# Performance work log

Measured on AMD Instinct MI355X. Metric: run time of the kernel, lower is better.

Reference implementation:

```python
import jax, jax.numpy as jnp
import numpy as np

B, N = 8, 1024
C = [256, 512, 1024]
C2 = C[1]
KV = sum(C)            # 1792
H = 4                  # num_attention_heads
EXPAND = 4
LN_EPS = 1e-6
IN_EPS = 1e-5          # nn.InstanceNorm2d default eps


def setup_inputs() -> dict:
    key = jax.random.key(0)
    ks = jax.random.split(key, 16)
    s = 0.02
    inp = {
        "emb1": jax.random.normal(ks[0], (B, N, C[0]), jnp.float32),
        "emb2": jax.random.normal(ks[1], (B, N, C[1]), jnp.float32),
        "emb3": jax.random.normal(ks[2], (B, N, C[2]), jnp.float32),
        # per-head projection weights stored as [in, out] (torch Linear applies x @ W.T)
        "Wq": jax.random.normal(ks[3], (H, C2, C2), jnp.float32) * s,
        "Wk": jax.random.normal(ks[4], (H, KV, KV), jnp.float32) * s,
        "Wv": jax.random.normal(ks[5], (H, KV, KV), jnp.float32) * s,
        "Wout": jax.random.normal(ks[6], (C2, C2), jnp.float32) * s,
        "ln1_g": jnp.ones((C2,), jnp.float32),
        "ln1_b": jnp.zeros((C2,), jnp.float32),
        "lnall_g": jnp.ones((KV,), jnp.float32),
        "lnall_b": jnp.zeros((KV,), jnp.float32),
        "lnffn_g": jnp.ones((C2,), jnp.float32),
        "lnffn_b": jnp.zeros((C2,), jnp.float32),
        "fc1_w": jax.random.normal(ks[7], (C2, C2 * EXPAND), jnp.float32) * s,
        "fc1_b": jnp.zeros((C2 * EXPAND,), jnp.float32),
        "fc2_w": jax.random.normal(ks[8], (C2 * EXPAND, C2), jnp.float32) * s,
        "fc2_b": jnp.zeros((C2,), jnp.float32),
    }
    return inp


def _layer_norm(x, g, b, eps=LN_EPS):
    m = jnp.mean(x, axis=-1, keepdims=True)
    v = jnp.var(x, axis=-1, keepdims=True)
    return (x - m) * jax.lax.rsqrt(v + eps) * g + b


def _instance_norm2d(x, eps=IN_EPS):
    # x: [B, H, C2, KV]; normalize each (B,H) map over its last two dims (no affine)
    m = jnp.mean(x, axis=(-2, -1), keepdims=True)
    v = jnp.var(x, axis=(-2, -1), keepdims=True)
    return (x - m) * jax.lax.rsqrt(v + eps)


def reference(emb1, emb2, emb3, Wq, Wk, Wv, Wout,
              ln1_g, ln1_b, lnall_g, lnall_b, lnffn_g, lnffn_b,
              fc1_w, fc1_b, fc2_w, fc2_b):
    org2 = emb2
    emb_all = jnp.concatenate([emb1, emb2, emb3], axis=2)        # [B,N,KV]
    cx2 = _layer_norm(emb2, ln1_g, ln1_b)                         # [B,N,C2]
    emb_all = _layer_norm(emb_all, lnall_g, lnall_b)              # [B,N,KV]

    # batched per-head projections (replaces the Python ModuleList loop)
    q = jnp.einsum('bnc,hcd->bhnd', cx2, Wq)                      # [B,H,N,C2]
    k = jnp.einsum('bnc,hcd->bhnd', emb_all, Wk)                  # [B,H,N,KV]
    v = jnp.einsum('bnc,hcd->bhnd', emb_all, Wv)                  # [B,H,N,KV]

    # channel attention: q^T k over the token axis
    scores = jnp.einsum('bhnc,bhnk->bhck', q, k) / np.sqrt(KV)    # [B,H,C2,KV]
    probs = jax.nn.softmax(_instance_norm2d(scores), axis=3)      # [B,H,C2,KV]

    # context = probs @ v^T, then mean over heads (fused into one einsum)
    ctx = jnp.einsum('bhck,bhnk->bnc', probs, v) / H              # [B,N,C2]
    o = ctx @ Wout                                                # [B,N,C2]

    cx2 = org2 + o
    x2 = _layer_norm(cx2, lnffn_g, lnffn_b)
    x2 = jax.nn.gelu(x2 @ fc1_w + fc1_b, approximate=False)
    x2 = x2 @ fc2_w + fc2_b
    return x2 + cx2
```

## Files before the change

### kernel.cpp

```cpp
#include <hip/hip_runtime.h>
#include <cstdint>
#include <cmath>

typedef __bf16 bf16_t;
typedef __attribute__((ext_vector_type(8))) __bf16 bf16x8;
typedef __attribute__((ext_vector_type(4))) float f32x4;

#define AS_G(x) ((__attribute__((address_space(1))) void*)(x))
#define AS_L(x) ((__attribute__((address_space(3))) void*)(x))

#define BK 64

#define BSZ 8
#define NTOK 1024
#define CC2 512
#define KVD 1792
#define NH 4
#define FFD 2048
#define ROWS 8192

#define BARM()   asm volatile("s_barrier" ::: "memory")
#define VMCNT8() asm volatile("s_waitcnt vmcnt(8)" ::: "memory")
#define VMCNT4() asm volatile("s_waitcnt vmcnt(4)" ::: "memory")
#define VMCNT0() asm volatile("s_waitcnt vmcnt(0)" ::: "memory")
#define LGKMD()  asm volatile("s_waitcnt lgkmcnt(0)" ::: "memory")


__device__ __forceinline__ void stage_pair(const bf16_t* __restrict__ A,
                                           const bf16_t* __restrict__ B,
                                           int ld, bf16_t* ldsA, bf16_t* ldsB, int tid)
{
#pragma unroll
  for (int it = 0; it < 4; ++it) {
    int chunk = it * 256 + tid;
    int r = chunk >> 3;
    int s = chunk & 7;
    int cg = ((s ^ (r & 7)) << 3);
    __builtin_amdgcn_global_load_lds(AS_G(A + (long)r * ld + cg),
                                     AS_L(ldsA + chunk * 8), 16, 0, 0);
    __builtin_amdgcn_global_load_lds(AS_G(B + (long)r * ld + cg),
                                     AS_L(ldsB + chunk * 8), 16, 0, 0);
  }
}

__device__ __forceinline__ void mfma_step(const bf16_t* ldsA, const bf16_t* ldsB,
                                          f32x4 acc[4][4], int wr, int wc, int lane, int kc)
{
  const int quad = lane >> 4, l16 = lane & 15;
  bf16x8 a[4], b[4];
#pragma unroll
  for (int i = 0; i < 4; ++i) {
    int r = wr * 64 + i * 16 + l16;
    int slot = (kc + quad) ^ (r & 7);
    a[i] = *(const bf16x8*)(ldsA + r * BK + slot * 8);
  }
#pragma unroll
  for (int j = 0; j < 4; ++j) {
    int r = wc * 64 + j * 16 + l16;
    int slot = (kc + quad) ^ (r & 7);
    b[j] = *(const bf16x8*)(ldsB + r * BK + slot * 8);
  }
#pragma unroll
  for (int i = 0; i < 4; ++i)
#pragma unroll
    for (int j = 0; j < 4; ++j)
      acc[i][j] = __builtin_amdgcn_mfma_f32_16x16x32_bf16(a[i], b[j], acc[i][j], 0, 0, 0);
}

#define GEMM_PROLOG() \
  __shared__ __align__(16) bf16_t ldsA[2][128 * BK]; \
  __shared__ __align__(16) bf16_t ldsB[2][128 * BK]; \
  const int tid = threadIdx.x; \
  const int wave = tid >> 6, lane = tid & 63; \
  const int wr = wave >> 1, wc = wave & 1; \
  f32x4 acc[4][4] = {};

#define GEMM_LOOP(Aptr, Bptr, Kdim) { \
  const bf16_t* Ap_ = (Aptr); const bf16_t* Bp_ = (Bptr); const int Kd_ = (Kdim); \
  const int nt_ = Kd_ / BK; \
  stage_pair(Ap_, Bp_, Kd_, ldsA[0], ldsB[0], tid); \
  for (int t = 0; t < nt_; ++t) { \
    const int cur = t & 1; \
    if (t + 1 < nt_) { \
      stage_pair(Ap_ + (t + 1) * BK, Bp_ + (t + 1) * BK, Kd_, ldsA[cur ^ 1], ldsB[cur ^ 1], tid); \
      VMCNT8(); \
    } else { VMCNT0(); } \
    BARM(); \
    mfma_step(ldsA[cur], ldsB[cur], acc, wr, wc, lane, 0); \
    mfma_step(ldsA[cur], ldsB[cur], acc, wr, wc, lane, 4); \
    LGKMD(); \
    BARM(); \
  } }

template <typename F>
__device__ __forceinline__ void epilogue_apply(f32x4 acc[4][4], int wr, int wc, int lane, F f)
{
  const int quad = lane >> 4, l16 = lane & 15;
#pragma unroll
  for (int i = 0; i < 4; ++i)
#pragma unroll
    for (int j = 0; j < 4; ++j)
#pragma unroll
      for (int r = 0; r < 4; ++r)
        f(wr * 64 + i * 16 + quad * 4 + r, wc * 64 + j * 16 + l16, acc[i][j][r]);
}


__device__ __forceinline__ void stage256h(const bf16_t* __restrict__ A,
                                          const bf16_t* __restrict__ B,
                                          int ld, bf16_t* ldsA, bf16_t* ldsB, int tid, int h)
{
#pragma unroll
  for (int i = 0; i < 2; ++i) {
    int it = h * 2 + i;
    int chunk = it * 512 + tid;
    int r = chunk >> 3;
    int s = chunk & 7;
    int cg = ((s ^ (r & 7)) << 3);
    __builtin_amdgcn_global_load_lds(AS_G(A + (long)r * ld + cg),
                                     AS_L(ldsA + chunk * 8), 16, 0, 0);
    __builtin_amdgcn_global_load_lds(AS_G(B + (long)r * ld + cg),
                                     AS_L(ldsB + chunk * 8), 16, 0, 0);
  }
}

__device__ __forceinline__ void qread_a(const bf16_t* ldsOp, int wr, int rh, int lane,
                                        bf16x8 a[4][2])
{
  const int quad = lane >> 4, l16 = lane & 15;
#pragma unroll
  for (int mi = 0; mi < 4; ++mi)
#pragma unroll
    for (int kc = 0; kc < 2; ++kc) {
      int r = wr * 128 + rh * 64 + mi * 16 + l16;
      int slot = (kc * 4 + quad) ^ (r & 7);
      a[mi][kc] = *(const bf16x8*)(ldsOp + r * BK + slot * 8);
    }
}

__device__ __forceinline__ void qread_b(const bf16_t* ldsOp, int wc, int ch, int lane,
                                        bf16x8 b[2][2])
{
  const int quad = lane >> 4, l16 = lane & 15;
#pragma unroll
  for (int nj = 0; nj < 2; ++nj)
#pragma unroll
    for (int kc = 0; kc < 2; ++kc) {
      int r = wc * 64 + ch * 32 + nj * 16 + l16;
      int slot = (kc * 4 + quad) ^ (r & 7);
      b[nj][kc] = *(const bf16x8*)(ldsOp + r * BK + slot * 8);
    }
}

template <int RH, int CH>
__device__ __forceinline__ void mfma16(f32x4 acc[8][4], const bf16x8 a[4][2],
                                       const bf16x8 (&b)[2][2])
{
#pragma unroll
  for (int mi = 0; mi < 4; ++mi)
#pragma unroll
    for (int nj = 0; nj < 2; ++nj)
#pragma unroll
      for (int kc = 0; kc < 2; ++kc)
        acc[RH * 4 + mi][CH * 2 + nj] =
            __builtin_amdgcn_mfma_f32_16x16x32_bf16(a[mi][kc], b[nj][kc],
                                                    acc[RH * 4 + mi][CH * 2 + nj], 0, 0, 0);
}

#define GEMM256_PROLOG() \
  __shared__ __align__(16) bf16_t ldsA[2][256 * BK]; \
  __shared__ __align__(16) bf16_t ldsB[2][256 * BK]; \
  __shared__ float sred[16]; \
  (void)sred; \
  const int tid = threadIdx.x; \
  const int wave = tid >> 6, lane = tid & 63; \
  const int wr = wave >> 2, wc = wave & 3; \
  f32x4 acc[8][4] = {};

#define GEMM256_LOOP(Aptr, Bptr, Kdim) { \
  const bf16_t* Ap = (Aptr); const bf16_t* Bp = (Bptr); const int Kd = (Kdim); \
  const int nt = Kd / BK; \
  stage256h(Ap, Bp, Kd, ldsA[0], ldsB[0], tid, 0); \
  stage256h(Ap, Bp, Kd, ldsA[0], ldsB[0], tid, 1); \
  for (int t = 0; t < nt; ++t) { \
    const int cur = t & 1; \
    if (t + 1 < nt) { \
      stage256h(Ap + (t + 1) * BK, Bp + (t + 1) * BK, Kd, ldsA[cur ^ 1], ldsB[cur ^ 1], tid, 0); \
      VMCNT4(); \
    } else { VMCNT0(); } \
    BARM(); \
    { \
      bf16x8 a[4][2], b0[2][2], b1[2][2]; \
      qread_a(ldsA[cur], wr, 0, lane, a); \
      qread_b(ldsB[cur], wc, 0, lane, b0); \
      qread_b(ldsB[cur], wc, 1, lane, b1); \
      mfma16<0, 0>(acc, a, b0); \
      mfma16<0, 1>(acc, a, b1); \
      if (t + 1 < nt) \
        stage256h(Ap + (t + 1) * BK, Bp + (t + 1) * BK, Kd, ldsA[cur ^ 1], ldsB[cur ^ 1], tid, 1); \
      qread_a(ldsA[cur], wr, 1, lane, a); \
      mfma16<1, 0>(acc, a, b0); \
      mfma16<1, 1>(acc, a, b1); \
    } \
    LGKMD(); \
    BARM(); \
  } }

template <typename F>
__device__ __forceinline__ void epi256(f32x4 acc[8][4], int wr, int wc, int lane, F f)
{
  const int quad = lane >> 4, l16 = lane & 15;
#pragma unroll
  for (int i = 0; i < 8; ++i)
#pragma unroll
    for (int j = 0; j < 4; ++j)
#pragma unroll
      for (int r = 0; r < 4; ++r)
        f(wr * 128 + (i >> 2) * 64 + (i & 3) * 16 + quad * 4 + r,
          wc * 64 + (j >> 1) * 32 + (j & 1) * 16 + l16, acc[i][j][r]);
}

__device__ __forceinline__ void swzA(int mg, int& bx, int& by, int& bz)
{
  int lid = blockIdx.x + 2 * (blockIdx.y + 7 * blockIdx.z);
  int xcd = lid & 7, s = lid >> 3;
  int y = s % 7, t = s / 7;
  bx = t & 1;
  by = y;
  if (mg) bz = (xcd >> 1) * 8 + (xcd & 1) * 4 + (t >> 1);
  else    bz = (xcd >> 2) * 8 + (xcd & 3) * 2 + (t >> 1);
}


__global__ void zstats_k(float* s)
{
  if (threadIdx.x < 64) s[threadIdx.x] = 0.f;
}

__global__ __launch_bounds__(256) void tconv_k(const float* __restrict__ in,
                                               bf16_t* __restrict__ out, int R, int Cc)
{
  __shared__ float tile[32][33];
  const long base = (long)blockIdx.z * R * Cc;
  const int c0 = blockIdx.x * 32, r0 = blockIdx.y * 32;
  const int tx = threadIdx.x & 31, ty = threadIdx.x >> 5;
#pragma unroll
  for (int i = 0; i < 4; ++i)
    tile[ty + i * 8][tx] = in[base + (long)(r0 + ty + i * 8) * Cc + c0 + tx];
  __syncthreads();
#pragma unroll
  for (int i = 0; i < 4; ++i)
    out[base + (long)(c0 + ty + i * 8) * R + r0 + tx] = (bf16_t)tile[tx][ty + i * 8];
}

__global__ __launch_bounds__(256) void tconv_bf_k(const bf16_t* __restrict__ in,
                                                  bf16_t* __restrict__ out, int R, int Cc)
{
  __shared__ float tile[32][33];
  const long base = (long)blockIdx.z * R * Cc;
  const int c0 = blockIdx.x * 32, r0 = blockIdx.y * 32;
  const int tx = threadIdx.x & 31, ty = threadIdx.x >> 5;
#pragma unroll
  for (int i = 0; i < 4; ++i)
    tile[ty + i * 8][tx] = (float)in[base + (long)(r0 + ty + i * 8) * Cc + c0 + tx];
  __syncthreads();
#pragma unroll
  for (int i = 0; i < 4; ++i)
    out[base + (long)(c0 + ty + i * 8) * R + r0 + tx] = (bf16_t)tile[tx][ty + i * 8];
}

__global__ __launch_bounds__(256) void cast_k(const float* __restrict__ in,
                                              bf16_t* __restrict__ out, long n)
{
  long i = ((long)blockIdx.x * 256 + threadIdx.x) * 4;
  if (i + 3 < n) {
    float4 v = *(const float4*)(in + i);
    out[i] = (bf16_t)v.x; out[i + 1] = (bf16_t)v.y;
    out[i + 2] = (bf16_t)v.z; out[i + 3] = (bf16_t)v.w;
  }
}

__global__ __launch_bounds__(256) void msum_add_k(const bf16_t* __restrict__ M,
                                                  bf16_t* __restrict__ O, int nfold)
{
  const long SLICE = (long)8 * CC2 * KVD;
  long i = ((long)blockIdx.x * 256 + threadIdx.x) * 8;
  float acc[8] = {};
  for (int h = 0; h < nfold; ++h) {
    bf16x8 x = *(const bf16x8*)(M + h * SLICE + i);
#pragma unroll
    for (int j = 0; j < 8; ++j) acc[j] += (float)x[j];
  }
  bf16x8 r;
#pragma unroll
  for (int j = 0; j < 8; ++j) r[j] = (bf16_t)acc[j];
  *(bf16x8*)(O + i) = r;
}

__global__ __launch_bounds__(256) void ln_concat_k(const float* __restrict__ e1,
                                                   const float* __restrict__ e2,
                                                   const float* __restrict__ e3,
                                                   const float* __restrict__ g1,
                                                   const float* __restrict__ b1,
                                                   const float* __restrict__ ga,
                                                   const float* __restrict__ ba,
                                                   bf16_t* __restrict__ cxln,
                                                   bf16_t* __restrict__ embln)
{
  const long row = blockIdx.x;
  const float* p1 = e1 + row * 256;
  const float* p2 = e2 + row * 512;
  const float* p3 = e3 + row * 1024;
  const int t = threadIdx.x;
  float vals[7];
  float sa = 0.f, qa = 0.f;
#pragma unroll
  for (int i = 0; i < 7; ++i) {
    int idx = t + i * 256;
    float x = (idx < 256) ? p1[idx] : (idx < 768 ? p2[idx - 256] : p3[idx - 768]);
    vals[i] = x;
    sa += x; qa += x * x;
  }
  float s2 = vals[1] + vals[2];
  float q2 = vals[1] * vals[1] + vals[2] * vals[2];
  for (int off = 32; off; off >>= 1) {
    sa += __shfl_down(sa, off, 64); qa += __shfl_down(qa, off, 64);
    s2 += __shfl_down(s2, off, 64); q2 += __shfl_down(q2, off, 64);
  }
  __shared__ float red[4][4];
  const int wave = t >> 6, lane = t & 63;
  if (lane == 0) { red[0][wave] = sa; red[1][wave] = qa; red[2][wave] = s2; red[3][wave] = q2; }
  __syncthreads();
  float SA = red[0][0] + red[0][1] + red[0][2] + red[0][3];
  float QA = red[1][0] + red[1][1] + red[1][2] + red[1][3];
  float S2 = red[2][0] + red[2][1] + red[2][2] + red[2][3];
  float Q2 = red[3][0] + red[3][1] + red[3][2] + red[3][3];
  float ma = SA * (1.f / 1792.f);
  float va = QA * (1.f / 1792.f) - ma * ma;
  float rsa = rsqrtf(va + 1e-6f);
  float m2 = S2 * (1.f / 512.f);
  float v2 = Q2 * (1.f / 512.f) - m2 * m2;
  float rs2 = rsqrtf(v2 + 1e-6f);
#pragma unroll
  for (int i = 0; i < 7; ++i) {
    int idx = t + i * 256;
    embln[row * 1792 + idx] = (bf16_t)((vals[i] - ma) * rsa * ga[idx] + ba[idx]);
  }
  cxln[row * 512 + t]       = (bf16_t)((vals[1] - m2) * rs2 * g1[t] + b1[t]);
  cxln[row * 512 + t + 256] = (bf16_t)((vals[2] - m2) * rs2 * g1[t + 256] + b1[t + 256]);
}

__global__ __launch_bounds__(256) void ln2_k(const float* __restrict__ X,
                                             const float* __restrict__ g,
                                             const float* __restrict__ bb,
                                             bf16_t* __restrict__ Y)
{
  const long row = blockIdx.x;
  const float* p = X + row * 512;
  const int t = threadIdx.x;
  float x0 = p[t], x1 = p[t + 256];
  float s = x0 + x1, q = x0 * x0 + x1 * x1;
  for (int off = 32; off; off >>= 1) {
    s += __shfl_down(s, off, 64); q += __shfl_down(q, off, 64);
  }
  __shared__ float red[2][4];
  const int wave = t >> 6, lane = t & 63;
  if (lane == 0) { red[0][wave] = s; red[1][wave] = q; }
  __syncthreads();
  float S = red[0][0] + red[0][1] + red[0][2] + red[0][3];
  float Q = red[1][0] + red[1][1] + red[1][2] + red[1][3];
  float m = S * (1.f / 512.f);
  float v = Q * (1.f / 512.f) - m * m;
  float rs = rsqrtf(v + 1e-6f);
  Y[row * 512 + t]       = (bf16_t)((x0 - m) * rs * g[t] + bb[t]);
  Y[row * 512 + t + 256] = (bf16_t)((x1 - m) * rs * g[t + 256] + bb[t + 256]);
}

__global__ __launch_bounds__(256) void softmax_k(bf16_t* __restrict__ SC,
                                                 const float* __restrict__ stats)
{
  const long rowid = blockIdx.x;
  const int z = (int)(rowid >> 9);
  const float inv_cnt = 1.f / (512.f * 1792.f);
  float m = stats[2 * z] * inv_cnt;
  float var = stats[2 * z + 1] * inv_cnt - m * m;
  float rs = rsqrtf(var + 1e-5f);
  bf16_t* rowp = SC + rowid * 1792;
  const int t = threadIdx.x;
  float v[7];
  float mx = -1e30f;
#pragma unroll
  for (int i = 0; i < 7; ++i) {
    v[i] = (float)rowp[t + i * 256] * rs;
    mx = fmaxf(mx, v[i]);
  }
  for (int off = 32; off; off >>= 1) mx = fmaxf(mx, __shfl_down(mx, off, 64));
  __shared__ float red[8];
  const int wave = t >> 6, lane = t & 63;
  if (lane == 0) red[wave] = mx;
  __syncthreads();
  mx = fmaxf(fmaxf(red[0], red[1]), fmaxf(red[2], red[3]));
  float sum = 0.f;
#pragma unroll
  for (int i = 0; i < 7; ++i) { v[i] = __expf(v[i] - mx); sum += v[i]; }
  for (int off = 32; off; off >>= 1) sum += __shfl_down(sum, off, 64);
  if (lane == 0) red[4 + wave] = sum;
  __syncthreads();
  float inv = 1.f / (red[4] + red[5] + red[6] + red[7]);
#pragma unroll
  for (int i = 0; i < 7; ++i) rowp[t + i * 256] = (bf16_t)(v[i] * inv);
}


__global__ __launch_bounds__(256) void gemm_ab(const bf16_t* __restrict__ A, long astride,
                                               const bf16_t* __restrict__ B, long bstride,
                                               bf16_t* __restrict__ C, long cstride,
                                               int K, int ldc)
{
  const int z = blockIdx.z;
  GEMM_PROLOG();
  const bf16_t* Ap = A + z * astride + (long)blockIdx.x * 128 * K;
  const bf16_t* Bp = B + z * bstride + (long)blockIdx.y * 128 * K;
  GEMM_LOOP(Ap, Bp, K);
  bf16_t* Cb = C + (long)z * cstride;
  const int rbase = blockIdx.x * 128, cbase = blockIdx.y * 128;
  epilogue_apply(acc, wr, wc, lane, [&](int rr, int cc, float v) {
    Cb[(long)(rbase + rr) * ldc + cbase + cc] = (bf16_t)v;
  });
}

__global__ __launch_bounds__(512, 2) void gemm_t1_256(const bf16_t* __restrict__ WqT,
                                                      const bf16_t* __restrict__ Gt,
                                                      bf16_t* __restrict__ T1, int mg)
{
  int bxx, byy, bzz;
  swzA(mg, bxx, byy, bzz);
  const int z = bzz, hh = z >> 3, b = z & 7;
  GEMM256_PROLOG();
  const bf16_t* Ap0 = WqT + (long)hh * CC2 * CC2 + (long)bxx * 256 * CC2;
  const bf16_t* Bp0 = Gt + (long)b * KVD * CC2 + (long)byy * 256 * CC2;
  GEMM256_LOOP(Ap0, Bp0, CC2);
  bf16_t* Cb = T1 + (long)z * CC2 * KVD;
  const int rbase = bxx * 256, cbase = byy * 256;
  epi256(acc, wr, wc, lane, [&](int rr, int cc, float v) {
    Cb[(long)(rbase + rr) * KVD + cbase + cc] = (bf16_t)v;
  });
}

__global__ __launch_bounds__(512, 2) void gemm_scores_256(const bf16_t* __restrict__ T1,
                                                          const bf16_t* __restrict__ WkT,
                                                          bf16_t* __restrict__ SC,
                                                          float* __restrict__ stats, int mg)
{
  int bxx, byy, bzz;
  swzA(mg, bxx, byy, bzz);
  const int z = bzz, hh = z >> 3;
  GEMM256_PROLOG();
  const bf16_t* Ap0 = T1 + (long)z * CC2 * KVD + (long)bxx * 256 * KVD;
  const bf16_t* Bp0 = WkT + (long)hh * KVD * KVD + (long)byy * 256 * KVD;
  GEMM256_LOOP(Ap0, Bp0, KVD);
  const float scale = 0.02362277854f;
  bf16_t* Cb = SC + (long)z * CC2 * KVD;
  const int rbase = bxx * 256, cbase = byy * 256;
  float s = 0.f, q = 0.f;
  epi256(acc, wr, wc, lane, [&](int rr, int cc, float v) {
    v *= scale;
    Cb[(long)(rbase + rr) * KVD + cbase + cc] = (bf16_t)v;
    s += v; q += v * v;
  });
  for (int off = 32; off; off >>= 1) { s += __shfl_down(s, off, 64); q += __shfl_down(q, off, 64); }
  if (lane == 0) { sred[wave] = s; sred[8 + wave] = q; }
  __syncthreads();
  if (tid == 0) {
    float S = 0.f, Q = 0.f;
#pragma unroll
    for (int w = 0; w < 8; ++w) { S += sred[w]; Q += sred[8 + w]; }
    atomicAdd(&stats[2 * z], S);
    atomicAdd(&stats[2 * z + 1], Q);
  }
}

__global__ __launch_bounds__(512, 2) void gemm_macc_256(const bf16_t* __restrict__ P,
                                                        const bf16_t* __restrict__ WvB,
                                                        bf16_t* __restrict__ M,
                                                        int first, int mg)
{
  int bxx, byy, bzz;
  swzA(mg, bxx, byy, bzz);
  const int z = bzz, hh = z >> 3;
  GEMM256_PROLOG();
  const bf16_t* Ap0 = P + (long)z * CC2 * KVD + (long)bxx * 256 * KVD;
  const bf16_t* Bp0 = WvB + (long)hh * KVD * KVD + (long)byy * 256 * KVD;
  GEMM256_LOOP(Ap0, Bp0, KVD);
  bf16_t* Cb = M + (long)z * CC2 * KVD;
  const int rbase = bxx * 256, cbase = byy * 256;
  epi256(acc, wr, wc, lane, [&](int rr, int cc, float v) {
    long idx = (long)(rbase + rr) * KVD + cbase + cc;
    float prev = first ? 0.f : (float)Cb[idx];
    Cb[idx] = (bf16_t)(prev + v * 0.25f);
  });
}

__global__ __launch_bounds__(256) void gemm_ctx(const bf16_t* __restrict__ E,
                                                const bf16_t* __restrict__ Msum8,
                                                bf16_t* __restrict__ CTX)
{
  const int b = blockIdx.z;
  GEMM_PROLOG();
  const bf16_t* Ap = E + (long)b * NTOK * KVD + (long)blockIdx.x * 128 * KVD;
  const bf16_t* Bp = Msum8 + (long)b * CC2 * KVD + (long)blockIdx.y * 128 * KVD;
  GEMM_LOOP(Ap, Bp, KVD);
  bf16_t* Cb = CTX + (long)b * NTOK * CC2;
  const int rbase = blockIdx.x * 128, cbase = blockIdx.y * 128;
  epilogue_apply(acc, wr, wc, lane, [&](int rr, int cc, float v) {
    Cb[(long)(rbase + rr) * CC2 + cbase + cc] = (bf16_t)v;
  });
}

__global__ __launch_bounds__(256) void gemm_resid(const bf16_t* __restrict__ A,
                                                  const bf16_t* __restrict__ B,
                                                  const float* __restrict__ emb2,
                                                  float* __restrict__ CX2)
{
  GEMM_PROLOG();
  const bf16_t* Ap = A + (long)blockIdx.x * 128 * CC2;
  const bf16_t* Bp = B + (long)blockIdx.y * 128 * CC2;
  GEMM_LOOP(Ap, Bp, CC2);
  const int rbase = blockIdx.x * 128, cbase = blockIdx.y * 128;
  epilogue_apply(acc, wr, wc, lane, [&](int rr, int cc, float v) {
    long idx = (long)(rbase + rr) * CC2 + cbase + cc;
    CX2[idx] = v + emb2[idx];
  });
}

__global__ __launch_bounds__(512, 2) void gemm_gelu_256(const bf16_t* __restrict__ A,
                                                        const bf16_t* __restrict__ B,
                                                        const float* __restrict__ bias,
                                                        bf16_t* __restrict__ H)
{
  GEMM256_PROLOG();
  const bf16_t* Ap0 = A + (long)blockIdx.x * 256 * CC2;
  const bf16_t* Bp0 = B + (long)blockIdx.y * 256 * CC2;
  GEMM256_LOOP(Ap0, Bp0, CC2);
  const int rbase = blockIdx.x * 256, cbase = blockIdx.y * 256;
  epi256(acc, wr, wc, lane, [&](int rr, int cc, float v) {
    float x = v + bias[cbase + cc];
    float g = 0.5f * x * (1.0f + erff(x * 0.70710678118f));
    H[(long)(rbase + rr) * FFD + cbase + cc] = (bf16_t)g;
  });
}

__global__ __launch_bounds__(256) void gemm_out(const bf16_t* __restrict__ A,
                                                const bf16_t* __restrict__ B,
                                                const float* __restrict__ bias,
                                                const float* __restrict__ CX2,
                                                float* __restrict__ OUT)
{
  GEMM_PROLOG();
  const bf16_t* Ap = A + (long)blockIdx.x * 128 * FFD;
  const bf16_t* Bp = B + (long)blockIdx.y * 128 * FFD;
  GEMM_LOOP(Ap, Bp, FFD);
  const int rbase = blockIdx.x * 128, cbase = blockIdx.y * 128;
  epilogue_apply(acc, wr, wc, lane, [&](int rr, int cc, float v) {
    long idx = (long)(rbase + rr) * CC2 + cbase + cc;
    OUT[idx] = v + bias[cbase + cc] + CX2[idx];
  });
}


extern "C" void kernel_launch(void* const* d_in, const int* in_sizes, int n_in,
                              void* d_out, int out_size, void* d_ws, size_t ws_size,
                              hipStream_t stream)
{
  const float* emb1   = (const float*)d_in[0];
  const float* emb2   = (const float*)d_in[1];
  const float* emb3   = (const float*)d_in[2];
  const float* Wq     = (const float*)d_in[3];
  const float* Wk     = (const float*)d_in[4];
  const float* Wv     = (const float*)d_in[5];
  const float* Wout   = (const float*)d_in[6];
  const float* ln1_g  = (const float*)d_in[7];
  const float* ln1_b  = (const float*)d_in[8];
  const float* lnall_g = (const float*)d_in[9];
  const float* lnall_b = (const float*)d_in[10];
  const float* lnffn_g = (const float*)d_in[11];
  const float* lnffn_b = (const float*)d_in[12];
  const float* fc1_w  = (const float*)d_in[13];
  const float* fc1_b  = (const float*)d_in[14];
  const float* fc2_w  = (const float*)d_in[15];
  const float* fc2_b  = (const float*)d_in[16];
  float* out = (float*)d_out;
  (void)in_sizes; (void)n_in; (void)out_size;

  const bool merged = ws_size >= (size_t)306 * 1000 * 1000;
  const int nheads = merged ? 4 : 2;
  const int nz = merged ? 32 : 16;
  const int nmslot = merged ? 32 : 16;

  char* ws = (char*)d_ws;
  size_t off = 0;
  auto alloc = [&](size_t bytes) {
    size_t r = off;
    off = (off + bytes + 255) & ~(size_t)255;
    return r;
  };

  size_t oEMBLN = alloc((size_t)ROWS * KVD * 2);
  size_t oCXLN  = alloc((size_t)ROWS * CC2 * 2);
  size_t oCX2   = alloc((size_t)ROWS * CC2 * 4);
  size_t oGt    = alloc((size_t)BSZ * KVD * CC2 * 2);
  size_t oMsum  = alloc((size_t)nmslot * CC2 * KVD * 2);
  size_t oWOT   = alloc((size_t)CC2 * CC2 * 2);
  size_t oF1T   = alloc((size_t)FFD * CC2 * 2);
  size_t oF2T   = alloc((size_t)CC2 * FFD * 2);
  size_t oSTATS = alloc(64 * 4);
  size_t oSCR   = alloc(0);
  size_t oCXLNT  = alloc((size_t)BSZ * CC2 * NTOK * 2);
  size_t oEMBLNT = alloc((size_t)BSZ * KVD * NTOK * 2);

  bf16_t* EMBLN  = (bf16_t*)(ws + oEMBLN);
  bf16_t* CXLN   = (bf16_t*)(ws + oCXLN);
  float*  CX2    = (float*)(ws + oCX2);
  bf16_t* Gt     = (bf16_t*)(ws + oGt);
  bf16_t* Msum   = (bf16_t*)(ws + oMsum);
  bf16_t* WOT    = (bf16_t*)(ws + oWOT);
  bf16_t* F1T    = (bf16_t*)(ws + oF1T);
  bf16_t* F2T    = (bf16_t*)(ws + oF2T);
  float*  STATS  = (float*)(ws + oSTATS);
  bf16_t* CXLNT  = (bf16_t*)(ws + oCXLNT);
  bf16_t* EMBLNT = (bf16_t*)(ws + oEMBLNT);

  char* scr = ws + oSCR;
  auto rnd = [](size_t v) { return (v + 255) & ~(size_t)255; };
  bf16_t* WqT = (bf16_t*)(scr);
  bf16_t* WkT = (bf16_t*)(scr + rnd((size_t)nheads * CC2 * CC2 * 2));
  bf16_t* WvB = (bf16_t*)((char*)WkT + rnd((size_t)nheads * KVD * KVD * 2));
  bf16_t* T1  = (bf16_t*)((char*)WvB + rnd((size_t)nheads * KVD * KVD * 2));
  bf16_t* SC  = (bf16_t*)((char*)T1 + rnd((size_t)nz * CC2 * KVD * 2));
  bf16_t* Msum8 = (bf16_t*)(scr);
  bf16_t* CTX   = (bf16_t*)(scr + rnd((size_t)8 * CC2 * KVD * 2));
  bf16_t* FFNH  = (bf16_t*)((char*)CTX + rnd((size_t)ROWS * CC2 * 2));
  bf16_t* X2LN = CXLN;

  zstats_k<<<1, 64, 0, stream>>>(STATS);
  tconv_k<<<dim3(16, 16), 256, 0, stream>>>(Wout, WOT, 512, 512);
  tconv_k<<<dim3(64, 16), 256, 0, stream>>>(fc1_w, F1T, 512, 2048);
  tconv_k<<<dim3(16, 64), 256, 0, stream>>>(fc2_w, F2T, 2048, 512);

  ln_concat_k<<<8192, 256, 0, stream>>>(emb1, emb2, emb3, ln1_g, ln1_b,
                                        lnall_g, lnall_b, CXLN, EMBLN);

  tconv_bf_k<<<dim3(16, 32, 8), 256, 0, stream>>>(CXLN, CXLNT, 1024, 512);
  tconv_bf_k<<<dim3(56, 32, 8), 256, 0, stream>>>(EMBLN, EMBLNT, 1024, 1792);
  gemm_ab<<<dim3(14, 4, 8), 256, 0, stream>>>(EMBLNT, (long)KVD * NTOK,
                                              CXLNT, (long)CC2 * NTOK,
                                              Gt, (long)KVD * CC2, NTOK, CC2);

  if (merged) {
    tconv_k<<<dim3(16, 16, 4), 256, 0, stream>>>(Wq, WqT, 512, 512);
    tconv_k<<<dim3(56, 56, 4), 256, 0, stream>>>(Wk, WkT, 1792, 1792);
    cast_k<<<12544, 256, 0, stream>>>(Wv, WvB, (long)4 * KVD * KVD);

    gemm_t1_256<<<dim3(2, 7, 32), 512, 0, stream>>>(WqT, Gt, T1, 1);
    gemm_scores_256<<<dim3(2, 7, 32), 512, 0, stream>>>(T1, WkT, SC, STATS, 1);
    softmax_k<<<16384, 256, 0, stream>>>(SC, STATS);
    gemm_macc_256<<<dim3(2, 7, 32), 512, 0, stream>>>(SC, WvB, Msum, 1, 1);
    msum_add_k<<<3584, 256, 0, stream>>>(Msum, Msum8, 4);
  } else {
    for (int g = 0; g < 2; ++g) {
      tconv_k<<<dim3(16, 16, 2), 256, 0, stream>>>(Wq + (long)g * 2 * CC2 * CC2, WqT, 512, 512);
      tconv_k<<<dim3(56, 56, 2), 256, 0, stream>>>(Wk + (long)g * 2 * KVD * KVD, WkT, 1792, 1792);
      cast_k<<<6272, 256, 0, stream>>>(Wv + (long)g * 2 * KVD * KVD, WvB, (long)2 * KVD * KVD);

      gemm_t1_256<<<dim3(2, 7, 16), 512, 0, stream>>>(WqT, Gt, T1, 0);
      gemm_scores_256<<<dim3(2, 7, 16), 512, 0, stream>>>(T1, WkT, SC, STATS + g * 32, 0);
      softmax_k<<<8192, 256, 0, stream>>>(SC, STATS + g * 32);
      gemm_macc_256<<<dim3(2, 7, 16), 512, 0, stream>>>(SC, WvB, Msum, g == 0 ? 1 : 0, 0);
    }
    msum_add_k<<<3584, 256, 0, stream>>>(Msum, Msum8, 2);
  }

  gemm_ctx<<<dim3(8, 4, 8), 256, 0, stream>>>(EMBLN, Msum8, CTX);

  gemm_resid<<<dim3(64, 4), 256, 0, stream>>>(CTX, WOT, emb2, CX2);

  ln2_k<<<8192, 256, 0, stream>>>(CX2, lnffn_g, lnffn_b, X2LN);
  gemm_gelu_256<<<dim3(32, 8), 512, 0, stream>>>(X2LN, F1T, fc1_b, FFNH);
  gemm_out<<<dim3(64, 4), 256, 0, stream>>>(FFNH, F2T, fc2_b, CX2, out);
}
```

Measured before the change: 745.3 us.

## Fuse softmax normalization into value GEMM A-operand loading

The softmax kernel now only computes per-row max and inverse sum and stores them in a small side buffer. The exponentiation and normalization are applied to the A fragments inside the macc GEMM after they are read from LDS. This removes a full write pass over the score matrix. In exchange it adds exp work inside the GEMM inner loop, recomputed for every column tile, plus register pressure from the per-row stats.

```diff
diff --git a/kernel.cpp b/kernel.cpp
--- a/kernel.cpp
+++ b/kernel.cpp
@@ -165,6 +165,18 @@
         acc[RH * 4 + mi][CH * 2 + nj] =
             __builtin_amdgcn_mfma_f32_16x16x32_bf16(a[mi][kc], b[nj][kc],
                                                     acc[RH * 4 + mi][CH * 2 + nj], 0, 0, 0);
+}
+
+__device__ __forceinline__ void pexp(bf16x8 a[4][2], const float* mxr, const float* invr,
+                                     float rs)
+{
+#pragma unroll
+  for (int mi = 0; mi < 4; ++mi)
+#pragma unroll
+    for (int kc = 0; kc < 2; ++kc)
+#pragma unroll
+      for (int j = 0; j < 8; ++j)
+        a[mi][kc][j] = (bf16_t)(__expf((float)a[mi][kc][j] * rs - mxr[mi]) * invr[mi]);
 }
 
 #define GEMM256_PROLOG() \
@@ -376,8 +388,9 @@
   Y[row * 512 + t + 256] = (bf16_t)((x1 - m) * rs * g[t + 256] + bb[t + 256]);
 }
 
-__global__ __launch_bounds__(256) void softmax_k(bf16_t* __restrict__ SC,
-                                                 const float* __restrict__ stats)
+__global__ __launch_bounds__(256) void sstats_k(const bf16_t* __restrict__ SC,
+                                                const float* __restrict__ stats,
+                                                float* __restrict__ srow)
 {
   const long rowid = blockIdx.x;
   const int z = (int)(rowid >> 9);
@@ -385,7 +398,7 @@
   float m = stats[2 * z] * inv_cnt;
   float var = stats[2 * z + 1] * inv_cnt - m * m;
   float rs = rsqrtf(var + 1e-5f);
-  bf16_t* rowp = SC + rowid * 1792;
+  const bf16_t* rowp = SC + rowid * 1792;
   const int t = threadIdx.x;
   float v[7];
   float mx = -1e30f;
@@ -402,13 +415,14 @@
   mx = fmaxf(fmaxf(red[0], red[1]), fmaxf(red[2], red[3]));
   float sum = 0.f;
 #pragma unroll
-  for (int i = 0; i < 7; ++i) { v[i] = __expf(v[i] - mx); sum += v[i]; }
+  for (int i = 0; i < 7; ++i) sum += __expf(v[i] - mx);
   for (int off = 32; off; off >>= 1) sum += __shfl_down(sum, off, 64);
   if (lane == 0) red[4 + wave] = sum;
   __syncthreads();
-  float inv = 1.f / (red[4] + red[5] + red[6] + red[7]);
-#pragma unroll
-  for (int i = 0; i < 7; ++i) rowp[t + i * 256] = (bf16_t)(v[i] * inv);
+  if (t == 0) {
+    srow[rowid * 2]     = mx;
+    srow[rowid * 2 + 1] = 1.f / (red[4] + red[5] + red[6] + red[7]);
+  }
 }
 
 
@@ -482,6 +496,8 @@
 
 __global__ __launch_bounds__(512, 2) void gemm_macc_256(const bf16_t* __restrict__ P,
                                                         const bf16_t* __restrict__ WvB,
+                                                        const float* __restrict__ stats,
+                                                        const float* __restrict__ srow,
                                                         bf16_t* __restrict__ M,
                                                         int first, int mg)
 {
@@ -489,9 +505,50 @@
   swzA(mg, bxx, byy, bzz);
   const int z = bzz, hh = z >> 3;
   GEMM256_PROLOG();
-  const bf16_t* Ap0 = P + (long)z * CC2 * KVD + (long)bxx * 256 * KVD;
-  const bf16_t* Bp0 = WvB + (long)hh * KVD * KVD + (long)byy * 256 * KVD;
-  GEMM256_LOOP(Ap0, Bp0, KVD);
+  const float inv_cnt = 1.f / (512.f * 1792.f);
+  float sm = stats[2 * z] * inv_cnt;
+  float var = stats[2 * z + 1] * inv_cnt - sm * sm;
+  float rs = rsqrtf(var + 1e-5f);
+  const int ll16 = lane & 15;
+  float mxr[2][4], invr[2][4];
+#pragma unroll
+  for (int rh = 0; rh < 2; ++rh)
+#pragma unroll
+    for (int mi = 0; mi < 4; ++mi) {
+      long rr = (long)z * 512 + bxx * 256 + wr * 128 + rh * 64 + mi * 16 + ll16;
+      mxr[rh][mi]  = srow[rr * 2];
+      invr[rh][mi] = srow[rr * 2 + 1];
+    }
+  const bf16_t* Ap = P + (long)z * CC2 * KVD + (long)bxx * 256 * KVD;
+  const bf16_t* Bp = WvB + (long)hh * KVD * KVD + (long)byy * 256 * KVD;
+  const int nt = KVD / BK;
+  stage256h(Ap, Bp, KVD, ldsA[0], ldsB[0], tid, 0);
+  stage256h(Ap, Bp, KVD, ldsA[0], ldsB[0], tid, 1);
+  for (int t = 0; t < nt; ++t) {
+    const int cur = t & 1;
+    if (t + 1 < nt) {
+      stage256h(Ap + (t + 1) * BK, Bp + (t + 1) * BK, KVD, ldsA[cur ^ 1], ldsB[cur ^ 1], tid, 0);
+      VMCNT4();
+    } else { VMCNT0(); }
+    BARM();
+    {
+      bf16x8 a[4][2], b0[2][2], b1[2][2];
+      qread_a(ldsA[cur], wr, 0, lane, a);
+      qread_b(ldsB[cur], wc, 0, lane, b0);
+      qread_b(ldsB[cur], wc, 1, lane, b1);
+      pexp(a, mxr[0], invr[0], rs);
+      mfma16<0, 0>(acc, a, b0);
+      mfma16<0, 1>(acc, a, b1);
+      if (t + 1 < nt)
+        stage256h(Ap + (t + 1) * BK, Bp + (t + 1) * BK, KVD, ldsA[cur ^ 1], ldsB[cur ^ 1], tid, 1);
+      qread_a(ldsA[cur], wr, 1, lane, a);
+      pexp(a, mxr[1], invr[1], rs);
+      mfma16<1, 0>(acc, a, b0);
+      mfma16<1, 1>(acc, a, b1);
+    }
+    LGKMD();
+    BARM();
+  }
   bf16_t* Cb = M + (long)z * CC2 * KVD;
   const int rbase = bxx * 256, cbase = byy * 256;
   epi256(acc, wr, wc, lane, [&](int rr, int cc, float v) {
@@ -614,6 +671,7 @@
   size_t oF1T   = alloc((size_t)FFD * CC2 * 2);
   size_t oF2T   = alloc((size_t)CC2 * FFD * 2);
   size_t oSTATS = alloc(64 * 4);
+  size_t oSROW  = alloc((size_t)32 * 512 * 2 * 4);
   size_t oSCR   = alloc(0);
   size_t oCXLNT  = alloc((size_t)BSZ * CC2 * NTOK * 2);
   size_t oEMBLNT = alloc((size_t)BSZ * KVD * NTOK * 2);
@@ -627,6 +685,7 @@
   bf16_t* F1T    = (bf16_t*)(ws + oF1T);
   bf16_t* F2T    = (bf16_t*)(ws + oF2T);
   float*  STATS  = (float*)(ws + oSTATS);
+  float*  SROW   = (float*)(ws + oSROW);
   bf16_t* CXLNT  = (bf16_t*)(ws + oCXLNT);
   bf16_t* EMBLNT = (bf16_t*)(ws + oEMBLNT);
 
@@ -663,8 +722,8 @@
 
     gemm_t1_256<<<dim3(2, 7, 32), 512, 0, stream>>>(WqT, Gt, T1, 1);
     gemm_scores_256<<<dim3(2, 7, 32), 512, 0, stream>>>(T1, WkT, SC, STATS, 1);
-    softmax_k<<<16384, 256, 0, stream>>>(SC, STATS);
-    gemm_macc_256<<<dim3(2, 7, 32), 512, 0, stream>>>(SC, WvB, Msum, 1, 1);
+    sstats_k<<<16384, 256, 0, stream>>>(SC, STATS, SROW);
+    gemm_macc_256<<<dim3(2, 7, 32), 512, 0, stream>>>(SC, WvB, STATS, SROW, Msum, 1, 1);
     msum_add_k<<<3584, 256, 0, stream>>>(Msum, Msum8, 4);
   } else {
     for (int g = 0; g < 2; ++g) {
@@ -674,8 +733,9 @@
 
       gemm_t1_256<<<dim3(2, 7, 16), 512, 0, stream>>>(WqT, Gt, T1, 0);
       gemm_scores_256<<<dim3(2, 7, 16), 512, 0, stream>>>(T1, WkT, SC, STATS + g * 32, 0);
-      softmax_k<<<8192, 256, 0, stream>>>(SC, STATS + g * 32);
-      gemm_macc_256<<<dim3(2, 7, 16), 512, 0, stream>>>(SC, WvB, Msum, g == 0 ? 1 : 0, 0);
+      sstats_k<<<8192, 256, 0, stream>>>(SC, STATS + g * 32, SROW);
+      gemm_macc_256<<<dim3(2, 7, 16), 512, 0, stream>>>(SC, WvB, STATS + g * 32, SROW,
+                                                        Msum, g == 0 ? 1 : 0, 0);
     }
     msum_add_k<<<3584, 256, 0, stream>>>(Msum, Msum8, 2);
   }
```

New measurement: 1.170 ms. 56.9% more time.
